# Performance work log

Hardware: AMD Instinct MI355X
Metric: run time of the kernel (lower is better)

Reference implementation:

```python
import jax, jax.numpy as jnp
import numpy as np

B, T, C, H = 4, 2048, 1024, 16
D = C // H          # head_dim = 64
FF = 2 * C          # ff_mult = 2
EPS = 1e-5


def _layernorm(x, g, b):
    mu = jnp.mean(x, axis=-1, keepdims=True)
    var = jnp.mean((x - mu) ** 2, axis=-1, keepdims=True)
    return (x - mu) * jax.lax.rsqrt(var + EPS) * g + b


def setup_inputs() -> dict:
    key = jax.random.key(0)
    ks = jax.random.split(key, 8)
    x = jax.random.normal(ks[0], (B, T, C), dtype=jnp.float32)
    perm = jax.random.permutation(ks[1], T).astype(jnp.int32)
    s_c = 1.0 / np.sqrt(C)
    s_f = 1.0 / np.sqrt(FF)
    Wqkv = jax.random.normal(ks[2], (C, 3 * C), dtype=jnp.float32) * s_c
    Wproj = jax.random.normal(ks[3], (C, C), dtype=jnp.float32) * s_c
    bproj = jnp.zeros((C,), dtype=jnp.float32)
    ln1_g = jnp.ones((C,), dtype=jnp.float32)
    ln1_b = jnp.zeros((C,), dtype=jnp.float32)
    ln2_g = jnp.ones((C,), dtype=jnp.float32)
    ln2_b = jnp.zeros((C,), dtype=jnp.float32)
    Wff1 = jax.random.normal(ks[4], (C, FF), dtype=jnp.float32) * s_c
    bff1 = jnp.zeros((FF,), dtype=jnp.float32)
    Wff2 = jax.random.normal(ks[5], (FF, C), dtype=jnp.float32) * s_f
    bff2 = jnp.zeros((C,), dtype=jnp.float32)
    return {"x": x, "perm": perm, "Wqkv": Wqkv, "Wproj": Wproj, "bproj": bproj,
            "ln1_g": ln1_g, "ln1_b": ln1_b, "ln2_g": ln2_g, "ln2_b": ln2_b,
            "Wff1": Wff1, "bff1": bff1, "Wff2": Wff2, "bff2": bff2}


def reference(x, perm, Wqkv, Wproj, bproj, ln1_g, ln1_b, ln2_g, ln2_b,
              Wff1, bff1, Wff2, bff2):
    # --- attention branch ---
    h = _layernorm(x, ln1_g, ln1_b)                       # [B,T,C]
    qkv = (h @ Wqkv).reshape(B, T, 3, H, D)
    q, k, v = qkv[:, :, 0], qkv[:, :, 1], qkv[:, :, 2]    # [B,T,H,D]
    # random-permuted causal additive mask: masked = ~tril[:, perm]
    rows = jnp.arange(T)[:, None]
    masked = perm[None, :] > rows                          # [T,T] bool
    bias = jnp.where(masked, -jnp.inf, 0.0).astype(x.dtype)
    scale = 1.0 / np.sqrt(D)
    scores = jnp.einsum('bqhd,bkhd->bhqk', q, k) * scale + bias
    attn = jax.nn.softmax(scores, axis=-1)                 # [B,H,T,T]
    y = jnp.einsum('bhqk,bkhd->bqhd', attn, v).reshape(B, T, C)
    x = x + y @ Wproj + bproj
    # --- MLP branch ---
    h2 = _layernorm(x, ln2_g, ln2_b)
    ff = jax.nn.gelu(h2 @ Wff1 + bff1, approximate=False) @ Wff2 + bff2
    return x + ff
```

## Files before the change

### kernel.cpp

```cpp
#include <hip/hip_runtime.h>
#include <math.h>

#define Bb 4
#define Tt 2048
#define Cc 1024
#define Hh 16
#define Dd 64
#define FFf 2048
#define Mrows (Bb*Tt)

typedef _Float16 f16;
typedef _Float16 half8 __attribute__((ext_vector_type(8)));
typedef _Float16 half4 __attribute__((ext_vector_type(4)));
typedef _Float16 half2 __attribute__((ext_vector_type(2)));
typedef float floatx4 __attribute__((ext_vector_type(4)));
typedef float floatx16 __attribute__((ext_vector_type(16)));

#define MFMA16(a,b,c)    __builtin_amdgcn_mfma_f32_16x16x32_f16(a,b,c,0,0,0)
#define MFMA16K16(a,b,c) __builtin_amdgcn_mfma_f32_16x16x16f16(a,b,c,0,0,0)
#define MFMA32(a,b,c)    __builtin_amdgcn_mfma_f32_32x32x16_f16(a,b,c,0,0,0)

__device__ __forceinline__ void g2l16(const void* g, void* l) {
  __builtin_amdgcn_global_load_lds((__attribute__((address_space(1))) void*)(g),
                                   (__attribute__((address_space(3))) void*)(l),
                                   16, 0, 0);
}

__global__ __launch_bounds__(256) void wt_ln_kernel(
    const float* __restrict__ Wqkv, const float* __restrict__ Wproj,
    const float* __restrict__ Wff1, const float* __restrict__ Wff2,
    f16* __restrict__ WqkvT, f16* __restrict__ WprojT,
    f16* __restrict__ Wff1T, f16* __restrict__ Wff2T,
    const float* __restrict__ x, const float* __restrict__ gam,
    const float* __restrict__ bet, f16* __restrict__ lnout) {
  const int tid = threadIdx.x;
  if (blockIdx.x < 8192) {
    __shared__ float tile[32][33];
    int idx = blockIdx.x;
    const float* W; f16* WT; int K, N, n0, k0;
    if (idx < 3072)      { W = Wqkv;  WT = WqkvT;  K = Cc;  N = 3*Cc; n0 = (idx % 96)*32; k0 = (idx / 96)*32; }
    else if (idx < 4096) { idx -= 3072; W = Wproj; WT = WprojT; K = Cc;  N = Cc;  n0 = (idx % 32)*32; k0 = (idx / 32)*32; }
    else if (idx < 6144) { idx -= 4096; W = Wff1;  WT = Wff1T;  K = Cc;  N = FFf; n0 = (idx % 64)*32; k0 = (idx / 64)*32; }
    else                 { idx -= 6144; W = Wff2;  WT = Wff2T;  K = FFf; N = Cc;  n0 = (idx % 32)*32; k0 = (idx / 32)*32; }
    const int tx = tid & 31, ty = tid >> 5;
    #pragma unroll
    for (int i = 0; i < 4; i++)
      tile[ty + 8*i][tx] = W[(size_t)(k0 + ty + 8*i) * N + n0 + tx];
    __syncthreads();
    #pragma unroll
    for (int i = 0; i < 4; i++)
      WT[(size_t)(n0 + ty + 8*i) * K + k0 + tx] = (f16)tile[tx][ty + 8*i];
  } else {
    const int row = blockIdx.x - 8192;
    const float4 v = ((const float4*)(x + (size_t)row * Cc))[tid];
    float s  = v.x + v.y + v.z + v.w;
    float ss = v.x*v.x + v.y*v.y + v.z*v.z + v.w*v.w;
    #pragma unroll
    for (int o = 32; o >= 1; o >>= 1) { s += __shfl_xor(s, o); ss += __shfl_xor(ss, o); }
    __shared__ float ps[4], pss[4];
    if ((tid & 63) == 0) { ps[tid >> 6] = s; pss[tid >> 6] = ss; }
    __syncthreads();
    s  = ps[0] + ps[1] + ps[2] + ps[3];
    ss = pss[0] + pss[1] + pss[2] + pss[3];
    const float mu   = s * (1.0f / Cc);
    const float rstd = rsqrtf(ss * (1.0f / Cc) - mu * mu + 1e-5f);
    const float4 g4 = ((const float4*)gam)[tid];
    const float4 b4 = ((const float4*)bet)[tid];
    half4 o;
    o[0] = (f16)((v.x - mu) * rstd * g4.x + b4.x);
    o[1] = (f16)((v.y - mu) * rstd * g4.y + b4.y);
    o[2] = (f16)((v.z - mu) * rstd * g4.z + b4.z);
    o[3] = (f16)((v.w - mu) * rstd * g4.w + b4.w);
    ((half4*)(lnout + (size_t)row * Cc))[tid] = o;
  }
}

__global__ __launch_bounds__(256) void ln_kernel(const float* __restrict__ x,
                                                 const float* __restrict__ gam,
                                                 const float* __restrict__ bet,
                                                 f16* __restrict__ out) {
  const int row = blockIdx.x;
  const int tid = threadIdx.x;
  const float4 v = ((const float4*)(x + (size_t)row * Cc))[tid];
  float s  = v.x + v.y + v.z + v.w;
  float ss = v.x*v.x + v.y*v.y + v.z*v.z + v.w*v.w;
  #pragma unroll
  for (int o = 32; o >= 1; o >>= 1) { s += __shfl_xor(s, o); ss += __shfl_xor(ss, o); }
  __shared__ float ps[4], pss[4];
  if ((tid & 63) == 0) { ps[tid >> 6] = s; pss[tid >> 6] = ss; }
  __syncthreads();
  s  = ps[0] + ps[1] + ps[2] + ps[3];
  ss = pss[0] + pss[1] + pss[2] + pss[3];
  const float mu   = s * (1.0f / Cc);
  const float rstd = rsqrtf(ss * (1.0f / Cc) - mu * mu + 1e-5f);
  const float4 g4 = ((const float4*)gam)[tid];
  const float4 b4 = ((const float4*)bet)[tid];
  half4 o;
  o[0] = (f16)((v.x - mu) * rstd * g4.x + b4.x);
  o[1] = (f16)((v.y - mu) * rstd * g4.y + b4.y);
  o[2] = (f16)((v.z - mu) * rstd * g4.z + b4.z);
  o[3] = (f16)((v.w - mu) * rstd * g4.w + b4.w);
  ((half4*)(out + (size_t)row * Cc))[tid] = o;
}

template <int MODE>
__device__ __forceinline__ void gemm_epilogue_tile(
    const floatx16& a, int rowBase, int col, int khalf,
    const float* __restrict__ resid, const float* __restrict__ bias,
    float* __restrict__ outF, f16* __restrict__ outH,
    f16* __restrict__ outQ, f16* __restrict__ outK, f16* __restrict__ outV) {
  if (MODE == 0) {
    const int s = col >> 10;
    const int hh = (col >> 6) & 15;
    const int d = col & 63;
    #pragma unroll
    for (int g = 0; g < 4; g++) {
      const int row0 = rowBase + 4*khalf + 8*g;
      const int bI = row0 >> 11;
      const int t0 = row0 & 2047;
      if (s == 2) {
        const size_t addr = (((size_t)(bI*Hh + hh)) * Dd + d) * Tt +
                            (t0 & ~63) + ((t0 >> 2) & 3)*16 + ((t0 >> 4) & 3)*4;
        half4 o;
        #pragma unroll
        for (int r = 0; r < 4; r++) o[r] = (f16)a[g*4 + r];
        *(half4*)&outV[addr] = o;
      } else {
        f16* dst = (s == 0) ? outQ : outK;
        const float sc = (s == 0) ? 0.18033688f : 1.0f;
        #pragma unroll
        for (int r = 0; r < 4; r++)
          dst[(((size_t)(bI*Hh + hh)) * Tt + t0 + r) * Dd + d] = (f16)(a[g*4 + r] * sc);
      }
    }
  } else {
    #pragma unroll
    for (int g = 0; g < 4; g++) {
      #pragma unroll
      for (int r = 0; r < 4; r++) {
        const int row = rowBase + 4*khalf + 8*g + r;
        const float vv = a[g*4 + r];
        if (MODE == 1) {
          const size_t ad = (size_t)row * Cc + col;
          outF[ad] = vv + resid[ad] + bias[col];
        } else if (MODE == 2) {
          const float t = vv + bias[col];
          const float gl = 0.5f * t * (1.0f + erff(t * 0.70710678118654752f));
          outH[(size_t)row * FFf + col] = (f16)gl;
        } else {
          const size_t ad = (size_t)row * Cc + col;
          outF[ad] = vv + bias[col] + resid[ad];
        }
      }
    }
  }
}

template <int MODE>
__global__ __launch_bounds__(256, 4) void gemm_kernel(
    const f16* __restrict__ A, const f16* __restrict__ Bt, const int Kdim,
    const float* __restrict__ resid, const float* __restrict__ bias,
    float* __restrict__ outF, f16* __restrict__ outH,
    f16* __restrict__ outQ, f16* __restrict__ outK, f16* __restrict__ outV) {
  __shared__ f16 As[128 * 64];
  __shared__ f16 Bs[128 * 64];
  const int tid = threadIdx.x;
  const int lane = tid & 63;
  const int w = tid >> 6;
  const int wr = w >> 1, wc = w & 1;

  const int Mb = gridDim.y;
  const int fid = blockIdx.y * gridDim.x + blockIdx.x;
  const int xcd = fid & 7;
  const int slot = fid >> 3;
  const int bn = xcd + 8 * (slot / Mb);
  const int bm = slot % Mb;

  floatx16 acc[2][2] = {};

  const int srow = lane >> 3;
  const int scol = ((lane & 7) ^ srow) * 8;
  const size_t aBase = (size_t)(bm*128 + w*32 + srow) * Kdim + scol;
  const size_t bBase = (size_t)(bn*128 + w*32 + srow) * Kdim + scol;

  const int m0 = wr*64 + (lane & 31);
  const int n0 = wc*64 + (lane & 31);
  const int khalf = lane >> 5;
  const int mx = (lane & 7);

  for (int ks = 0; ks < Kdim; ks += 64) {
    __syncthreads();
    #pragma unroll
    for (int c = 0; c < 4; c++) {
      g2l16(A  + aBase + (size_t)(c*8)*Kdim + ks, &As[(w*32 + c*8) * 64]);
      g2l16(Bt + bBase + (size_t)(c*8)*Kdim + ks, &Bs[(w*32 + c*8) * 64]);
    }
    __syncthreads();
    #pragma unroll
    for (int kk = 0; kk < 4; kk++) {
      const int kg = kk*2 + khalf;
      half8 aF[2], bF[2];
      aF[0] = *(const half8*)&As[(m0     ) * 64 + ((kg ^ mx) * 8)];
      aF[1] = *(const half8*)&As[(m0 + 32) * 64 + ((kg ^ mx) * 8)];
      bF[0] = *(const half8*)&Bs[(n0     ) * 64 + ((kg ^ mx) * 8)];
      bF[1] = *(const half8*)&Bs[(n0 + 32) * 64 + ((kg ^ mx) * 8)];
      acc[0][0] = MFMA32(aF[0], bF[0], acc[0][0]);
      acc[0][1] = MFMA32(aF[0], bF[1], acc[0][1]);
      acc[1][0] = MFMA32(aF[1], bF[0], acc[1][0]);
      acc[1][1] = MFMA32(aF[1], bF[1], acc[1][1]);
    }
  }

  #pragma unroll
  for (int mi = 0; mi < 2; mi++)
    #pragma unroll
    for (int ni = 0; ni < 2; ni++)
      gemm_epilogue_tile<MODE>(acc[mi][ni], bm*128 + wr*64 + mi*32,
                               bn*128 + wc*64 + ni*32 + (lane & 31), khalf,
                               resid, bias, outF, outH, outQ, outK, outV);
}

__global__ __launch_bounds__(256, 4) void attn_kernel(
    const f16* __restrict__ Q, const f16* __restrict__ Kg,
    const f16* __restrict__ Vtp, const int* __restrict__ perm,
    f16* __restrict__ Y) {
  __shared__ f16 Ks[64 * 64];
  __shared__ f16 Vs[64 * 64];
  __shared__ int permS[64];

  const int tid = threadIdx.x;
  const int lane = tid & 63;
  const int w = tid >> 6;
  const int low = lane & 15;
  const int quad = lane >> 4;
  const int bh = blockIdx.y;
  const int q0 = blockIdx.x * 128;
  const int b = bh >> 4, h = bh & 15;

  half8 qF[2][2];
  {
    const size_t base = ((size_t)bh * Tt + q0 + w*32) * Dd;
    #pragma unroll
    for (int qi = 0; qi < 2; qi++)
      #pragma unroll
      for (int kc = 0; kc < 2; kc++)
        qF[qi][kc] = *(const half8*)(Q + base + (size_t)(qi*16 + low) * Dd +
                                     kc*32 + quad*8);
  }

  floatx4 O[4][2] = {};
  floatx4 Ol[2] = {};
  const half4 ones4 = {(f16)1.f, (f16)1.f, (f16)1.f, (f16)1.f};

  const int gd = ((lane & 7) ^ (lane >> 3)) * 8;
  const int krow = lane >> 3;

  for (int kt = 0; kt < Tt / 64; kt++) {
    const int kbase = kt * 64;
    __syncthreads();
    {
      const size_t kgBase = ((size_t)bh * Tt + kbase) * Dd;
      const size_t vgBase = ((size_t)bh * Dd) * Tt + kbase;
      g2l16(Kg  + kgBase + (size_t)(w*16 + 0 + krow) * Dd + gd, &Ks[(w*2 + 0) * 512]);
      g2l16(Kg  + kgBase + (size_t)(w*16 + 8 + krow) * Dd + gd, &Ks[(w*2 + 1) * 512]);
      g2l16(Vtp + vgBase + (size_t)(w*16 + 0 + krow) * Tt + gd, &Vs[(w*2 + 0) * 512]);
      g2l16(Vtp + vgBase + (size_t)(w*16 + 8 + krow) * Tt + gd, &Vs[(w*2 + 1) * 512]);
      if (tid < 64) permS[tid] = perm[kbase + tid];
    }
    __syncthreads();

    floatx4 S[2][4] = {};
    #pragma unroll
    for (int kc = 0; kc < 2; kc++) {
      #pragma unroll
      for (int ki = 0; ki < 4; ki++) {
        const int key = ki*16 + low;
        const half8 kf = *(const half8*)&Ks[key * 64 + (((kc*4 + quad) ^ (lane & 7)) * 8)];
        S[0][ki] = MFMA16(kf, qF[0][kc], S[0][ki]);
        S[1][ki] = MFMA16(kf, qF[1][kc], S[1][ki]);
      }
    }

    int4 pk[4];
    #pragma unroll
    for (int ki = 0; ki < 4; ki++) pk[ki] = *(const int4*)&permS[ki*16 + quad*4];

    half4 pF[2][4];
    #pragma unroll
    for (int qi = 0; qi < 2; qi++) {
      const int qrow = q0 + w*32 + qi*16 + low;
      #pragma unroll
      for (int ki = 0; ki < 4; ki++) {
        const floatx4 sv = S[qi][ki];
        const float p0 = (pk[ki].x > qrow) ? 0.f : __builtin_amdgcn_exp2f(sv[0]);
        const float p1 = (pk[ki].y > qrow) ? 0.f : __builtin_amdgcn_exp2f(sv[1]);
        const float p2 = (pk[ki].z > qrow) ? 0.f : __builtin_amdgcn_exp2f(sv[2]);
        const float p3 = (pk[ki].w > qrow) ? 0.f : __builtin_amdgcn_exp2f(sv[3]);
        const half2 lo = __builtin_bit_cast(half2, __builtin_amdgcn_cvt_pkrtz(p0, p1));
        const half2 hi = __builtin_bit_cast(half2, __builtin_amdgcn_cvt_pkrtz(p2, p3));
        pF[qi][ki] = __builtin_shufflevector(lo, hi, 0, 1, 2, 3);
      }
    }

    #pragma unroll
    for (int ki2 = 0; ki2 < 2; ki2++) {
      Ol[0] = MFMA16K16(ones4, pF[0][2*ki2 + 0], Ol[0]);
      Ol[1] = MFMA16K16(ones4, pF[1][2*ki2 + 0], Ol[1]);
      Ol[0] = MFMA16K16(ones4, pF[0][2*ki2 + 1], Ol[0]);
      Ol[1] = MFMA16K16(ones4, pF[1][2*ki2 + 1], Ol[1]);
      #pragma unroll
      for (int ni = 0; ni < 4; ni++) {
        const int d = ni*16 + low;
        const half8 v8 = *(const half8*)&Vs[d * 64 + (((quad*2 + ki2) ^ (lane & 7)) * 8)];
        const half4 vfA = __builtin_shufflevector(v8, v8, 0, 1, 2, 3);
        const half4 vfB = __builtin_shufflevector(v8, v8, 4, 5, 6, 7);
        O[ni][0] = MFMA16K16(vfA, pF[0][2*ki2 + 0], O[ni][0]);
        O[ni][1] = MFMA16K16(vfA, pF[1][2*ki2 + 0], O[ni][1]);
        O[ni][0] = MFMA16K16(vfB, pF[0][2*ki2 + 1], O[ni][0]);
        O[ni][1] = MFMA16K16(vfB, pF[1][2*ki2 + 1], O[ni][1]);
      }
    }
  }

  #pragma unroll
  for (int qi = 0; qi < 2; qi++) {
    const float linv = 1.0f / Ol[qi][0];
    const int trow = q0 + w*32 + qi*16 + low;
    #pragma unroll
    for (int ni = 0; ni < 4; ni++) {
      half4 o;
      #pragma unroll
      for (int r = 0; r < 4; r++) o[r] = (f16)(O[ni][qi][r] * linv);
      *(half4*)&Y[((size_t)(b * Tt + trow)) * Cc + h*64 + ni*16 + quad*4] = o;
    }
  }
}

extern "C" void kernel_launch(void* const* d_in, const int* in_sizes, int n_in,
                              void* d_out, int out_size, void* d_ws, size_t ws_size,
                              hipStream_t stream) {
  const float* x     = (const float*)d_in[0];
  const int*   perm  = (const int*)d_in[1];
  const float* Wqkv  = (const float*)d_in[2];
  const float* Wproj = (const float*)d_in[3];
  const float* bproj = (const float*)d_in[4];
  const float* ln1g  = (const float*)d_in[5];
  const float* ln1b  = (const float*)d_in[6];
  const float* ln2g  = (const float*)d_in[7];
  const float* ln2b  = (const float*)d_in[8];
  const float* Wff1  = (const float*)d_in[9];
  const float* bff1  = (const float*)d_in[10];
  const float* Wff2  = (const float*)d_in[11];
  const float* bff2  = (const float*)d_in[12];
  float* out = (float*)d_out;

  char* ws = (char*)d_ws;
  size_t off = 0;
  auto alloc = [&](size_t bytes) -> void* {
    void* p = ws + off;
    off += (bytes + 255) & ~(size_t)255;
    return p;
  };
  f16*   h1     = (f16*)alloc((size_t)Mrows * Cc * 2);
  f16*   qb     = (f16*)alloc((size_t)Mrows * Cc * 2);
  f16*   kb     = (f16*)alloc((size_t)Mrows * Cc * 2);
  f16*   vtp    = (f16*)alloc((size_t)Mrows * Cc * 2);
  f16*   yb     = (f16*)alloc((size_t)Mrows * Cc * 2);
  float* xa     = (float*)alloc((size_t)Mrows * Cc * 4);
  f16*   h2     = (f16*)alloc((size_t)Mrows * Cc * 2);
  f16*   gb     = (f16*)alloc((size_t)Mrows * FFf * 2);
  f16*   WqkvT  = (f16*)alloc((size_t)3 * Cc * Cc * 2);
  f16*   WprojT = (f16*)alloc((size_t)Cc * Cc * 2);
  f16*   Wff1T  = (f16*)alloc((size_t)FFf * Cc * 2);
  f16*   Wff2T  = (f16*)alloc((size_t)Cc * FFf * 2);

  wt_ln_kernel<<<16384, 256, 0, stream>>>(Wqkv, Wproj, Wff1, Wff2,
                                          WqkvT, WprojT, Wff1T, Wff2T,
                                          x, ln1g, ln1b, h1);

  gemm_kernel<0><<<dim3(3*Cc/128, Mrows/128), 256, 0, stream>>>(
      h1, WqkvT, Cc, nullptr, nullptr, nullptr, nullptr, qb, kb, vtp);

  attn_kernel<<<dim3(Tt/128, Bb*Hh), 256, 0, stream>>>(qb, kb, vtp, perm, yb);

  gemm_kernel<1><<<dim3(Cc/128, Mrows/128), 256, 0, stream>>>(
      yb, WprojT, Cc, x, bproj, xa, nullptr, nullptr, nullptr, nullptr);

  ln_kernel<<<Mrows, 256, 0, stream>>>(xa, ln2g, ln2b, h2);

  gemm_kernel<2><<<dim3(FFf/128, Mrows/128), 256, 0, stream>>>(
      h2, Wff1T, Cc, nullptr, bff1, nullptr, gb, nullptr, nullptr, nullptr);

  gemm_kernel<3><<<dim3(Cc/128, Mrows/128), 256, 0, stream>>>(
      gb, Wff2T, FFf, xa, bff2, out, nullptr, nullptr, nullptr, nullptr);
}
```

Before: 437.8 us.

## Reorder keys by inverse permutation to turn permuted mask into causal and skip tiles

Computes the inverse of the key permutation and uses it to gather rows of the LayerNorm output when producing K and V in the QKV GEMM, so keys sit in permuted order. The permuted mask then becomes an ordinary causal mask. The attention kernel can skip all key tiles beyond the diagonal and only apply the mask on diagonal tiles, and its grid is reordered to balance long and short query tiles. This removes about half of the attention work and the per-tile perm loads, at the cost of gathered row loads in the GEMM's A operand.

```diff
diff --git a/kernel.cpp b/kernel.cpp
--- a/kernel.cpp
+++ b/kernel.cpp
@@ -32,8 +32,14 @@
     f16* __restrict__ WqkvT, f16* __restrict__ WprojT,
     f16* __restrict__ Wff1T, f16* __restrict__ Wff2T,
     const float* __restrict__ x, const float* __restrict__ gam,
-    const float* __restrict__ bet, f16* __restrict__ lnout) {
+    const float* __restrict__ bet, f16* __restrict__ lnout,
+    const int* __restrict__ perm, int* __restrict__ inv) {
   const int tid = threadIdx.x;
+  if (blockIdx.x >= 16384) {
+    #pragma unroll
+    for (int i = tid; i < Tt; i += 256) inv[perm[i]] = i;
+    return;
+  }
   if (blockIdx.x < 8192) {
     __shared__ float tile[32][33];
     int idx = blockIdx.x;
@@ -161,7 +167,8 @@
     const f16* __restrict__ A, const f16* __restrict__ Bt, const int Kdim,
     const float* __restrict__ resid, const float* __restrict__ bias,
     float* __restrict__ outF, f16* __restrict__ outH,
-    f16* __restrict__ outQ, f16* __restrict__ outK, f16* __restrict__ outV) {
+    f16* __restrict__ outQ, f16* __restrict__ outK, f16* __restrict__ outV,
+    const int* __restrict__ inv) {
   __shared__ f16 As[128 * 64];
   __shared__ f16 Bs[128 * 64];
   const int tid = threadIdx.x;
@@ -180,7 +187,21 @@
 
   const int srow = lane >> 3;
   const int scol = ((lane & 7) ^ srow) * 8;
-  const size_t aBase = (size_t)(bm*128 + w*32 + srow) * Kdim + scol;
+  size_t aRow[4];
+  {
+    const int r0 = bm*128 + w*32 + srow;
+    if (MODE == 0 && bn >= 8) {
+      const int bI = r0 >> 11;
+      const int t0 = r0 & 2047;
+      #pragma unroll
+      for (int c = 0; c < 4; c++)
+        aRow[c] = (size_t)(bI*Tt + inv[t0 + c*8]) * Kdim + scol;
+    } else {
+      #pragma unroll
+      for (int c = 0; c < 4; c++)
+        aRow[c] = (size_t)(r0 + c*8) * Kdim + scol;
+    }
+  }
   const size_t bBase = (size_t)(bn*128 + w*32 + srow) * Kdim + scol;
 
   const int m0 = wr*64 + (lane & 31);
@@ -192,7 +213,7 @@
     __syncthreads();
     #pragma unroll
     for (int c = 0; c < 4; c++) {
-      g2l16(A  + aBase + (size_t)(c*8)*Kdim + ks, &As[(w*32 + c*8) * 64]);
+      g2l16(A  + aRow[c] + ks, &As[(w*32 + c*8) * 64]);
       g2l16(Bt + bBase + (size_t)(c*8)*Kdim + ks, &Bs[(w*32 + c*8) * 64]);
     }
     __syncthreads();
@@ -222,19 +243,19 @@
 
 __global__ __launch_bounds__(256, 4) void attn_kernel(
     const f16* __restrict__ Q, const f16* __restrict__ Kg,
-    const f16* __restrict__ Vtp, const int* __restrict__ perm,
-    f16* __restrict__ Y) {
+    const f16* __restrict__ Vtp, f16* __restrict__ Y) {
   __shared__ f16 Ks[64 * 64];
   __shared__ f16 Vs[64 * 64];
-  __shared__ int permS[64];
 
   const int tid = threadIdx.x;
   const int lane = tid & 63;
   const int w = tid >> 6;
   const int low = lane & 15;
   const int quad = lane >> 4;
-  const int bh = blockIdx.y;
-  const int q0 = blockIdx.x * 128;
+  const int bh = blockIdx.x;
+  const int y = blockIdx.y;
+  const int tile = (y & 12) + ((y & 3) ^ (y >> 2));
+  const int q0 = tile * 128;
   const int b = bh >> 4, h = bh & 15;
 
   half8 qF[2][2];
@@ -254,8 +275,9 @@
 
   const int gd = ((lane & 7) ^ (lane >> 3)) * 8;
   const int krow = lane >> 3;
-
-  for (int kt = 0; kt < Tt / 64; kt++) {
+  const int nkb = (q0 >> 6) + 2;
+
+  for (int kt = 0; kt < nkb; kt++) {
     const int kbase = kt * 64;
     __syncthreads();
     {
@@ -265,7 +287,6 @@
       g2l16(Kg  + kgBase + (size_t)(w*16 + 8 + krow) * Dd + gd, &Ks[(w*2 + 1) * 512]);
       g2l16(Vtp + vgBase + (size_t)(w*16 + 0 + krow) * Tt + gd, &Vs[(w*2 + 0) * 512]);
       g2l16(Vtp + vgBase + (size_t)(w*16 + 8 + krow) * Tt + gd, &Vs[(w*2 + 1) * 512]);
-      if (tid < 64) permS[tid] = perm[kbase + tid];
     }
     __syncthreads();
 
@@ -281,24 +302,39 @@
       }
     }
 
-    int4 pk[4];
-    #pragma unroll
-    for (int ki = 0; ki < 4; ki++) pk[ki] = *(const int4*)&permS[ki*16 + quad*4];
-
     half4 pF[2][4];
-    #pragma unroll
-    for (int qi = 0; qi < 2; qi++) {
-      const int qrow = q0 + w*32 + qi*16 + low;
-      #pragma unroll
-      for (int ki = 0; ki < 4; ki++) {
-        const floatx4 sv = S[qi][ki];
-        const float p0 = (pk[ki].x > qrow) ? 0.f : __builtin_amdgcn_exp2f(sv[0]);
-        const float p1 = (pk[ki].y > qrow) ? 0.f : __builtin_amdgcn_exp2f(sv[1]);
-        const float p2 = (pk[ki].z > qrow) ? 0.f : __builtin_amdgcn_exp2f(sv[2]);
-        const float p3 = (pk[ki].w > qrow) ? 0.f : __builtin_amdgcn_exp2f(sv[3]);
-        const half2 lo = __builtin_bit_cast(half2, __builtin_amdgcn_cvt_pkrtz(p0, p1));
-        const half2 hi = __builtin_bit_cast(half2, __builtin_amdgcn_cvt_pkrtz(p2, p3));
-        pF[qi][ki] = __builtin_shufflevector(lo, hi, 0, 1, 2, 3);
+    const bool needmask = (kbase + 63 > q0 + w*32);
+    if (needmask) {
+      #pragma unroll
+      for (int qi = 0; qi < 2; qi++) {
+        const int qrow = q0 + w*32 + qi*16 + low;
+        #pragma unroll
+        for (int ki = 0; ki < 4; ki++) {
+          const floatx4 sv = S[qi][ki];
+          const int kj = kbase + ki*16 + quad*4;
+          const float p0 = (kj + 0 > qrow) ? 0.f : __builtin_amdgcn_exp2f(sv[0]);
+          const float p1 = (kj + 1 > qrow) ? 0.f : __builtin_amdgcn_exp2f(sv[1]);
+          const float p2 = (kj + 2 > qrow) ? 0.f : __builtin_amdgcn_exp2f(sv[2]);
+          const float p3 = (kj + 3 > qrow) ? 0.f : __builtin_amdgcn_exp2f(sv[3]);
+          const half2 lo = __builtin_bit_cast(half2, __builtin_amdgcn_cvt_pkrtz(p0, p1));
+          const half2 hi = __builtin_bit_cast(half2, __builtin_amdgcn_cvt_pkrtz(p2, p3));
+          pF[qi][ki] = __builtin_shufflevector(lo, hi, 0, 1, 2, 3);
+        }
+      }
+    } else {
+      #pragma unroll
+      for (int qi = 0; qi < 2; qi++) {
+        #pragma unroll
+        for (int ki = 0; ki < 4; ki++) {
+          const floatx4 sv = S[qi][ki];
+          const float p0 = __builtin_amdgcn_exp2f(sv[0]);
+          const float p1 = __builtin_amdgcn_exp2f(sv[1]);
+          const float p2 = __builtin_amdgcn_exp2f(sv[2]);
+          const float p3 = __builtin_amdgcn_exp2f(sv[3]);
+          const half2 lo = __builtin_bit_cast(half2, __builtin_amdgcn_cvt_pkrtz(p0, p1));
+          const half2 hi = __builtin_bit_cast(half2, __builtin_amdgcn_cvt_pkrtz(p2, p3));
+          pF[qi][ki] = __builtin_shufflevector(lo, hi, 0, 1, 2, 3);
+        }
       }
     }
 
@@ -373,24 +409,25 @@
   f16*   WprojT = (f16*)alloc((size_t)Cc * Cc * 2);
   f16*   Wff1T  = (f16*)alloc((size_t)FFf * Cc * 2);
   f16*   Wff2T  = (f16*)alloc((size_t)Cc * FFf * 2);
-
-  wt_ln_kernel<<<16384, 256, 0, stream>>>(Wqkv, Wproj, Wff1, Wff2,
+  int*   inv    = (int*)alloc((size_t)Tt * 4);
+
+  wt_ln_kernel<<<16385, 256, 0, stream>>>(Wqkv, Wproj, Wff1, Wff2,
                                           WqkvT, WprojT, Wff1T, Wff2T,
-                                          x, ln1g, ln1b, h1);
+                                          x, ln1g, ln1b, h1, perm, inv);
 
   gemm_kernel<0><<<dim3(3*Cc/128, Mrows/128), 256, 0, stream>>>(
-      h1, WqkvT, Cc, nullptr, nullptr, nullptr, nullptr, qb, kb, vtp);
-
-  attn_kernel<<<dim3(Tt/128, Bb*Hh), 256, 0, stream>>>(qb, kb, vtp, perm, yb);
+      h1, WqkvT, Cc, nullptr, nullptr, nullptr, nullptr, qb, kb, vtp, inv);
+
+  attn_kernel<<<dim3(Bb*Hh, Tt/128), 256, 0, stream>>>(qb, kb, vtp, yb);
 
   gemm_kernel<1><<<dim3(Cc/128, Mrows/128), 256, 0, stream>>>(
-      yb, WprojT, Cc, x, bproj, xa, nullptr, nullptr, nullptr, nullptr);
+      yb, WprojT, Cc, x, bproj, xa, nullptr, nullptr, nullptr, nullptr, nullptr);
 
   ln_kernel<<<Mrows, 256, 0, stream>>>(xa, ln2g, ln2b, h2);
 
   gemm_kernel<2><<<dim3(FFf/128, Mrows/128), 256, 0, stream>>>(
-      h2, Wff1T, Cc, nullptr, bff1, nullptr, gb, nullptr, nullptr, nullptr);
+      h2, Wff1T, Cc, nullptr, bff1, nullptr, gb, nullptr, nullptr, nullptr, nullptr);
 
   gemm_kernel<3><<<dim3(Cc/128, Mrows/128), 256, 0, stream>>>(
-      gb, Wff2T, FFf, xa, bff2, out, nullptr, nullptr, nullptr, nullptr);
-}
+      gb, Wff2T, FFf, xa, bff2, out, nullptr, nullptr, nullptr, nullptr, nullptr);
+}
```

After: 435.7 us. Within noise of the previous version (-0.5%).
